# Optimization experiments

Measured on AMD Instinct MI355X. Metric: run time of the kernel, lower is better.

The kernel has to match this reference:

```python
import jax, jax.numpy as jnp
import numpy as np
import math

D_MODEL = 1024
D_STATE = 16
D_CONV = 4
EXPAND = 2
D_INNER = EXPAND * D_MODEL
DT_RANK = 64
BATCH = 4
SEQ_LEN = 2048


def setup_inputs() -> dict:
    key = jax.random.key(0)
    ks = jax.random.split(key, 10)
    hidden_states = jax.random.normal(ks[0], (BATCH, SEQ_LEN, D_MODEL), jnp.float32)
    in_proj_w = jax.random.normal(ks[1], (D_MODEL, 2 * D_INNER), jnp.float32) * (D_MODEL ** -0.5)
    conv_w = jax.random.normal(ks[2], (D_INNER, D_CONV), jnp.float32) * (D_CONV ** -0.5)
    conv_b = jnp.zeros((D_INNER,), jnp.float32)
    x_proj_w = jax.random.normal(ks[3], (D_INNER, DT_RANK + 2 * D_STATE), jnp.float32) * (D_INNER ** -0.5)
    dt_init_std = DT_RANK ** -0.5
    dt_proj_w = jax.random.uniform(ks[4], (DT_RANK, D_INNER), jnp.float32, -dt_init_std, dt_init_std)
    # inverse-softplus init of dt bias: dt ~ logUniform(dt_min, dt_max)
    dt_min, dt_max, dt_floor = 0.001, 0.1, 1e-4
    dt = jnp.exp(jax.random.uniform(ks[5], (D_INNER,), jnp.float32) * (math.log(dt_max) - math.log(dt_min)) + math.log(dt_min))
    dt = jnp.clip(dt, dt_floor, None)
    dt_proj_b = dt + jnp.log(-jnp.expm1(-dt))
    A = jnp.tile(jnp.arange(1, D_STATE + 1, dtype=jnp.float32)[None, :], (D_INNER, 1))
    A_log = jnp.log(A)
    D = jnp.ones((D_INNER,), jnp.float32)
    out_proj_w = jax.random.normal(ks[6], (D_INNER, D_MODEL), jnp.float32) * (D_INNER ** -0.5)
    return {
        "hidden_states": hidden_states,
        "in_proj_w": in_proj_w,
        "conv_w": conv_w,
        "conv_b": conv_b,
        "x_proj_w": x_proj_w,
        "dt_proj_w": dt_proj_w,
        "dt_proj_b": dt_proj_b,
        "A_log": A_log,
        "D": D,
        "out_proj_w": out_proj_w,
    }


def _mamba_forward(hidden_states, in_proj_w, conv_w, conv_b, x_proj_w, dt_proj_w, dt_proj_b, A_log, D, out_proj_w):
    b, L, _ = hidden_states.shape
    d_state = A_log.shape[1]
    dt_rank = dt_proj_w.shape[0]
    K = conv_w.shape[1]

    xz = hidden_states @ in_proj_w                     # (b, L, 2*d_inner)
    x, z = jnp.split(xz, 2, axis=-1)                   # each (b, L, d_inner)

    # causal depthwise conv1d (padding = K-1, truncated to L)
    x_pad = jnp.pad(x, ((0, 0), (K - 1, 0), (0, 0)))
    x = sum(x_pad[:, k:k + L, :] * conv_w[:, k] for k in range(K)) + conv_b
    x = jax.nn.silu(x)

    x_dbl = x @ x_proj_w                               # (b, L, dt_rank + 2*d_state)
    dt, B, C = jnp.split(x_dbl, [dt_rank, dt_rank + d_state], axis=-1)
    dt = jax.nn.softplus(dt @ dt_proj_w + dt_proj_b)   # (b, L, d_inner)
    A = -jnp.exp(A_log)                                # (d_inner, d_state)

    def step(h, inp):
        x_t, dt_t, B_t, C_t = inp                      # (b,d), (b,d), (b,n), (b,n)
        dA = jnp.exp(A[None] * dt_t[..., None])        # (b, d, n)
        h = dA * h + dt_t[..., None] * B_t[:, None, :] * x_t[..., None]
        y_t = jnp.einsum('bdn,bn->bd', h, C_t) + D * x_t
        return h, y_t

    h0 = jnp.zeros((b, x.shape[-1], d_state), x.dtype)
    xs = (x.transpose(1, 0, 2), dt.transpose(1, 0, 2), B.transpose(1, 0, 2), C.transpose(1, 0, 2))
    _, ys = jax.lax.scan(step, h0, xs)                 # ys: (L, b, d_inner)
    y = ys.transpose(1, 0, 2) * jax.nn.silu(z)
    return y @ out_proj_w                              # (b, L, d_model)


def reference(hidden_states, in_proj_w, conv_w, conv_b, x_proj_w, dt_proj_w, dt_proj_b, A_log, D, out_proj_w):
    return _mamba_forward(hidden_states, in_proj_w, conv_w, conv_b, x_proj_w, dt_proj_w, dt_proj_b, A_log, D, out_proj_w)
```

## Files before the change

### kernel.cpp

```cpp
#include <hip/hip_runtime.h>
#include <hip/hip_bf16.h>


#define DM 1024
#define DS 16
#define DC 4
#define DI 2048
#define DR 64
#define NB 4
#define SL 2048
#define NTOK (NB*SL)
#define XDBL_W (DR + 2*DS)
#define CONV_R 8

typedef __hip_bfloat16 bf16;
typedef unsigned short u16;
typedef __attribute__((ext_vector_type(8))) short s8v;
typedef __attribute__((ext_vector_type(4))) float f4v;
typedef __attribute__((ext_vector_type(2))) float f2v;
typedef __attribute__((ext_vector_type(4))) unsigned short us4;

__device__ __forceinline__ float b2f(bf16 v) { return __bfloat162float(v); }
__device__ __forceinline__ bf16  f2b(float v) { return __float2bfloat16(v); }
__device__ __forceinline__ u16 f2u(float x) {
    union { bf16 h; u16 s; } u; u.h = f2b(x); return u.s;
}
__device__ __forceinline__ float u2f(u16 s) {
    union { bf16 h; u16 s; } u; u.s = s; return b2f(u.h);
}

__device__ __forceinline__ bool sniff_bf16(const void* Dones) {
    return ((const u16*)Dones)[0] == 0x3F80u;
}

__device__ __forceinline__ float softplus_fast(float v) {
    return fmaxf(v, 0.f) + __logf(1.f + __expf(-fabsf(v)));
}

__device__ __forceinline__ float silu_fast(float v) {
    return v * __builtin_amdgcn_rcpf(1.f + __expf(-v));
}

template<int MODE>
__device__ __forceinline__ float ld(const void* p, size_t i, bool bf) {
    if (MODE == 0) return b2f(((const bf16*)p)[i]);
    if (MODE == 1) return ((const float*)p)[i];
    return bf ? b2f(((const bf16*)p)[i]) : ((const float*)p)[i];
}
template<int MODE>
__device__ __forceinline__ void st(void* p, size_t i, bool bf, float v) {
    if (MODE == 0)      { ((bf16*)p)[i] = f2b(v); }
    else if (MODE == 1) { ((float*)p)[i] = v; }
    else { if (bf) ((bf16*)p)[i] = f2b(v); else ((float*)p)[i] = v; }
}

template<int CM>
__device__ __forceinline__ void cstore(void* C, void* C2, size_t m, int n,
                                       int ldc, bool bf, float v) {
    if (CM == 3) {
        if (n < DR) ((bf16*)C2)[m * DR + n] = f2b(v);
        else        ((float*)C)[m * (2 * DS) + (n - DR)] = v;
    } else {
        st<CM>(C, m * (size_t)ldc + n, bf, v);
    }
}

#define AS1 __attribute__((address_space(1)))
#define AS3 __attribute__((address_space(3)))
__device__ __forceinline__ void gload_lds16(const void* g, void* l) {
    __builtin_amdgcn_global_load_lds((const AS1 unsigned int*)g,
                                     (AS3 unsigned int*)l, 16, 0, 0);
}

__global__ __launch_bounds__(256) void cast_bf16_kernel(
    const void* __restrict__ src, bf16* __restrict__ dst,
    const void* __restrict__ sniff)
{
    const bool bf = sniff_bf16(sniff);
    const size_t i = ((size_t)blockIdx.x * 256 + threadIdx.x) * 4;
    if (bf) {
        *(us4*)((u16*)dst + i) = *(const us4*)((const u16*)src + i);
    } else {
        const f4v f = *(const f4v*)((const float*)src + i);
        us4 o; o.x = f2u(f.x); o.y = f2u(f.y); o.z = f2u(f.z); o.w = f2u(f.w);
        *(us4*)((u16*)dst + i) = o;
    }
}

__global__ __launch_bounds__(256) void transpose_w(
    const void* __restrict__ w, bf16* __restrict__ wt,
    int K, int N, const void* __restrict__ sniff)
{
    const bool bf = sniff_bf16(sniff);
    __shared__ float t[32][33];
    const int tx = threadIdx.x & 31, ty = threadIdx.x >> 5;
    const int n0 = blockIdx.x * 32, k0 = blockIdx.y * 32;
    #pragma unroll
    for (int i = 0; i < 4; i++) {
        int k = k0 + ty + i * 8, n = n0 + tx;
        t[ty + i * 8][tx] = (n < N) ? ld<2>(w, (size_t)k * N + n, bf) : 0.f;
    }
    __syncthreads();
    #pragma unroll
    for (int i = 0; i < 4; i++) {
        int n = n0 + ty + i * 8, k = k0 + tx;
        wt[(size_t)n * K + k] = f2b(t[tx][ty + i * 8]);
    }
}

template<int BN, int CM>
__global__ __launch_bounds__(512, 1) void gemm_big(
    const bf16* __restrict__ A, int lda,
    const bf16* __restrict__ Bt,
    void* __restrict__ C, int ldc, int K,
    const void* __restrict__ sniff)
{
    constexpr int NF = BN / 128;
    constexpr int BH_ROWS = BN / 2;
    constexpr int BPASS = BH_ROWS / 64;
    constexpr int AH_B = 128 * 128;
    constexpr int BH_B = BH_ROWS * 128;

    const bool bf = sniff_bf16(sniff);
    __shared__ char AhL[2 * 2 * AH_B];
    __shared__ char BhL[2 * 2 * BH_B];

    const int tid = threadIdx.x, lane = tid & 63, wave = tid >> 6;
    const int wm = wave >> 2, wn = wave & 3;
    const int ll = lane & 15, qd = lane >> 4;
    const int swz = (ll & 7) << 4;

    const int m0 = blockIdx.x * 256, n0 = blockIdx.y * BN;

    const int s_r  = tid >> 3;
    const int s_cb = ((tid & 7) << 4) ^ ((s_r & 7) << 4);
    const char* Ab = (const char*)A;
    const char* Bb = (const char*)Bt;

#define STAGE_A(tt, hh) do {                                                  \
    char* _d = AhL + ((((tt) & 1) * 2 + (hh)) * AH_B);                        \
    _Pragma("unroll")                                                         \
    for (int _c = 0; _c < 2; ++_c) {                                          \
        const int _r = _c * 64 + s_r;                                         \
        gload_lds16(Ab + (((size_t)(m0 + (hh)*128 + _r) * lda + (tt)*64) << 1)\
                        + s_cb,                                               \
                    _d + _r * 128 + (tid & 7) * 16);                          \
    } } while (0)

#define STAGE_B(tt, hh) do {                                                  \
    char* _d = BhL + ((((tt) & 1) * 2 + (hh)) * BH_B);                        \
    _Pragma("unroll")                                                         \
    for (int _c = 0; _c < BPASS; ++_c) {                                      \
        const int _r = _c * 64 + s_r;                                         \
        gload_lds16(Bb + (((size_t)(n0 + (hh)*BH_ROWS + _r) * K + (tt)*64) << 1)\
                        + s_cb,                                               \
                    _d + _r * 128 + (tid & 7) * 16);                          \
    } } while (0)

#define WAIT_VC() do {                                                        \
    if constexpr (NF == 2) asm volatile("s_waitcnt vmcnt(4)" ::: "memory");   \
    else                   asm volatile("s_waitcnt vmcnt(3)" ::: "memory");   \
    } while (0)

    f4v acc[8][2 * NF];
    #pragma unroll
    for (int i = 0; i < 8; i++)
        #pragma unroll
        for (int j = 0; j < 2 * NF; j++) acc[i][j] = (f4v){0.f, 0.f, 0.f, 0.f};

    const int NT = K >> 6;
    STAGE_A(0, 0); STAGE_B(0, 0); STAGE_A(0, 1); STAGE_B(0, 1);
    STAGE_A(1, 0); STAGE_B(1, 0);
    WAIT_VC();
    __builtin_amdgcn_sched_barrier(0);
    __builtin_amdgcn_s_barrier();

    for (int t = 0; t < NT; ++t) {
        const int cur = t & 1;
        #pragma unroll
        for (int p = 0; p < 4; ++p) {
            const int mh = p >> 1, nh = p & 1;
            const char* Ah = AhL + (cur * 2 + mh) * AH_B;
            const char* Bh = BhL + (cur * 2 + nh) * BH_B;
            s8v af[4][2], bv[NF][2];
            #pragma unroll
            for (int fr = 0; fr < 4; ++fr)
                #pragma unroll
                for (int ks = 0; ks < 2; ++ks)
                    af[fr][ks] = *(const s8v*)(Ah + (wm*64 + fr*16 + ll) * 128
                                                  + ((ks*64 + qd*16) ^ swz));
            #pragma unroll
            for (int fn = 0; fn < NF; ++fn)
                #pragma unroll
                for (int ks = 0; ks < 2; ++ks)
                    bv[fn][ks] = *(const s8v*)(Bh + (wn*16*NF + fn*16 + ll) * 128
                                                  + ((ks*64 + qd*16) ^ swz));
            if (p == 0 && t + 1 < NT) STAGE_B(t + 1, 1);
            if (p == 1 && t + 1 < NT) STAGE_A(t + 1, 1);
            if (p == 2 && t + 2 < NT) STAGE_A(t + 2, 0);
            if (p == 3 && t + 2 < NT) STAGE_B(t + 2, 0);
            __builtin_amdgcn_sched_barrier(0);
            __builtin_amdgcn_s_barrier();
            asm volatile("s_waitcnt lgkmcnt(0)" ::: "memory");
            __builtin_amdgcn_sched_barrier(0);
            __builtin_amdgcn_s_setprio(1);
            #pragma unroll
            for (int fr = 0; fr < 4; ++fr)
                #pragma unroll
                for (int fn = 0; fn < NF; ++fn)
                    #pragma unroll
                    for (int ks = 0; ks < 2; ++ks)
                        acc[mh*4 + fr][nh*NF + fn] =
                            __builtin_amdgcn_mfma_f32_16x16x32_bf16(
                                af[fr][ks], bv[fn][ks],
                                acc[mh*4 + fr][nh*NF + fn], 0, 0, 0);
            __builtin_amdgcn_s_setprio(0);
            if (p == 3) WAIT_VC();
            __builtin_amdgcn_sched_barrier(0);
            __builtin_amdgcn_s_barrier();
        }
    }

    #pragma unroll
    for (int mh = 0; mh < 2; ++mh)
        #pragma unroll
        for (int fr = 0; fr < 4; ++fr)
            #pragma unroll
            for (int nh = 0; nh < 2; ++nh)
                #pragma unroll
                for (int fn = 0; fn < NF; ++fn) {
                    const int col = n0 + nh * (BN/2) + wn * 16 * NF + fn * 16 + ll;
                    #pragma unroll
                    for (int rr = 0; rr < 4; ++rr) {
                        const int row = m0 + mh * 128 + wm * 64 + fr * 16 + qd * 4 + rr;
                        st<CM>(C, (size_t)row * ldc + col, bf,
                               acc[mh*4 + fr][nh*NF + fn][rr]);
                    }
                }
#undef STAGE_A
#undef STAGE_B
#undef WAIT_VC
}

template<int CM, int EPI>
__global__ __launch_bounds__(256) void gemm_mfma(
    const bf16* __restrict__ A, int lda,
    const bf16* __restrict__ Bt,
    void* __restrict__ C, void* __restrict__ C2, int ldc,
    int M, int N, int K,
    const void* __restrict__ bias,
    const void* __restrict__ sniff)
{
    const bool bf = sniff_bf16(sniff);
    __shared__ short As[128 * 32];
    __shared__ short Bs[128 * 32];

    const int tid  = threadIdx.x;
    const int lane = tid & 63;
    const int wave = tid >> 6;
    const int wm = (wave & 1) * 64;
    const int wn = (wave >> 1) * 64;
    const int m0 = blockIdx.x * 128;
    const int n0 = blockIdx.y * 128;
    const int ll = lane & 15;
    const int qd = lane >> 4;

    const int srow  = lane >> 2;
    const int skoff = (lane & 3) * 8;

    const short* Ag = (const short*)A;
    const short* Bg = (const short*)Bt;
    char* AsB = (char*)As + wave * 2048 + lane * 16;
    char* BsB = (char*)Bs + wave * 2048 + lane * 16;
    const size_t a_row = (size_t)(m0 + wave * 32 + srow);
    const size_t b_row = (size_t)(n0 + wave * 32 + srow);

    f4v acc[4][4];
    #pragma unroll
    for (int i = 0; i < 4; i++)
        #pragma unroll
        for (int j = 0; j < 4; j++)
            acc[i][j] = (f4v){0.f, 0.f, 0.f, 0.f};

    for (int k0 = 0; k0 < K; k0 += 32) {
        gload_lds16(Ag + a_row * lda + k0 + skoff,            AsB);
        gload_lds16(Ag + (a_row + 16) * lda + k0 + skoff,     AsB + 1024);
        gload_lds16(Bg + b_row * K + k0 + skoff,              BsB);
        gload_lds16(Bg + (b_row + 16) * K + k0 + skoff,       BsB + 1024);
        __syncthreads();

        s8v af[4], bfr[4];
        #pragma unroll
        for (int s = 0; s < 4; s++)
            af[s] = *(const s8v*)&As[(wm + s * 16 + ll) * 32 + qd * 8];
        #pragma unroll
        for (int s = 0; s < 4; s++)
            bfr[s] = *(const s8v*)&Bs[(wn + s * 16 + ll) * 32 + qd * 8];
        #pragma unroll
        for (int i = 0; i < 4; i++)
            #pragma unroll
            for (int j = 0; j < 4; j++)
                acc[i][j] = __builtin_amdgcn_mfma_f32_16x16x32_bf16(
                    af[i], bfr[j], acc[i][j], 0, 0, 0);
        __syncthreads();
    }

    #pragma unroll
    for (int sn = 0; sn < 4; sn++) {
        const int cn = n0 + wn + sn * 16 + ll;
        if (cn >= N) continue;
        float bvv = 0.f;
        if (EPI == 1) bvv = ld<2>(bias, cn, bf);
        #pragma unroll
        for (int sm = 0; sm < 4; sm++) {
            #pragma unroll
            for (int r = 0; r < 4; r++) {
                const int cm = m0 + wm + sm * 16 + qd * 4 + r;
                float v = acc[sm][sn][r];
                if (EPI == 1) v = softplus_fast(v + bvv);
                cstore<CM>(C, C2, (size_t)cm, cn, ldc, bf, v);
            }
        }
    }
}

template<int AM, int CM, int EPI>
__global__ __launch_bounds__(256) void gemm_kernel(
    const void* __restrict__ A, int lda,
    const void* __restrict__ B, size_t bbase, int ldb,
    void* __restrict__ C, void* __restrict__ C2, int ldc,
    int M, int N, int K,
    const void* __restrict__ bias,
    const void* __restrict__ sniff)
{
    const bool bf = sniff_bf16(sniff);
    const int BM = 64, BN = 64, BK = 16;
    __shared__ float Asm[BK][BM + 4];
    __shared__ float Bsm[BK][BN + 4];

    const int tid = threadIdx.x;
    const int m0 = blockIdx.x * BM;
    const int n0 = blockIdx.y * BN;
    const int tx = tid % 16;
    const int ty = tid / 16;
    const int a_k = tid % BK;
    const int a_m = tid / BK;
    const int b_n = tid % BN;
    const int b_k = tid / BN;

    float acc[4][4] = {};

    for (int k0 = 0; k0 < K; k0 += BK) {
        #pragma unroll
        for (int i = 0; i < 4; i++) {
            int m = m0 + a_m + i * 16;
            float v = 0.f;
            if (m < M) v = ld<AM>(A, (size_t)m * lda + (k0 + a_k), bf);
            Asm[a_k][a_m + i * 16] = v;
        }
        #pragma unroll
        for (int i = 0; i < 4; i++) {
            int kk = b_k + i * 4;
            int n = n0 + b_n;
            float v = 0.f;
            if (n < N) v = ld<2>(B, bbase + (size_t)(k0 + kk) * ldb + n, bf);
            Bsm[kk][b_n] = v;
        }
        __syncthreads();
        #pragma unroll
        for (int kk = 0; kk < BK; kk++) {
            float av[4], bv[4];
            #pragma unroll
            for (int i = 0; i < 4; i++) av[i] = Asm[kk][ty * 4 + i];
            #pragma unroll
            for (int j = 0; j < 4; j++) bv[j] = Bsm[kk][tx * 4 + j];
            #pragma unroll
            for (int i = 0; i < 4; i++)
                #pragma unroll
                for (int j = 0; j < 4; j++)
                    acc[i][j] += av[i] * bv[j];
        }
        __syncthreads();
    }
    #pragma unroll
    for (int i = 0; i < 4; i++) {
        int m = m0 + ty * 4 + i;
        if (m >= M) continue;
        #pragma unroll
        for (int j = 0; j < 4; j++) {
            int n = n0 + tx * 4 + j;
            if (n >= N) continue;
            float v = acc[i][j];
            if (EPI == 1) {
                v += ld<2>(bias, n, bf);
                v = softplus_fast(v);
            }
            cstore<CM>(C, C2, (size_t)m, n, ldc, bf, v);
        }
    }
}

__global__ __launch_bounds__(256) void conv_silu_kernel(
    const bf16* __restrict__ xg, const void* __restrict__ w,
    const void* __restrict__ bias, bf16* __restrict__ xc,
    const void* __restrict__ sniff)
{
    const bool bf = sniff_bf16(sniff);
    const int c  = blockIdx.x * 256 + threadIdx.x;
    const int r0 = blockIdx.y * CONV_R;
    const int l0 = r0 % SL;

    float w0, w1, w2, w3;
    if (bf) {
        const us4 wv = *(const us4*)((const u16*)w + (size_t)c * 4);
        w0 = u2f(wv.x); w1 = u2f(wv.y); w2 = u2f(wv.z); w3 = u2f(wv.w);
    } else {
        const f4v wv = *(const f4v*)((const float*)w + (size_t)c * 4);
        w0 = wv.x; w1 = wv.y; w2 = wv.z; w3 = wv.w;
    }
    const float bs = ld<2>(bias, c, bf);

    float xm3 = (l0 >= 3) ? b2f(xg[(size_t)(r0 - 3) * DI + c]) : 0.f;
    float xm2 = (l0 >= 2) ? b2f(xg[(size_t)(r0 - 2) * DI + c]) : 0.f;
    float xm1 = (l0 >= 1) ? b2f(xg[(size_t)(r0 - 1) * DI + c]) : 0.f;

    #pragma unroll
    for (int i = 0; i < CONV_R; i++) {
        const size_t row = (size_t)(r0 + i);
        const float x0 = b2f(xg[row * DI + c]);
        const float acc = bs + w0 * xm3 + w1 * xm2 + w2 * xm1 + w3 * x0;
        const float s = acc / (1.f + __expf(-acc));
        xc[row * DI + c] = f2b(s);
        xm3 = xm2; xm2 = xm1; xm1 = x0;
    }
}

__global__ __launch_bounds__(256) void scan_pass1(
    const bf16* __restrict__ xc, const bf16* __restrict__ dt,
    const float* __restrict__ bc,
    const void* __restrict__ A_log, const void* __restrict__ Dones,
    float* __restrict__ P, float* __restrict__ Q, int nch)
{
    const bool bf = sniff_bf16(Dones);
    const int tid = threadIdx.x;
    const int d = blockIdx.x * 256 + tid;
    const int c = blockIdx.y;
    const int b = blockIdx.z;
    const int T = SL / nch;
    __shared__ u16 xs[32 * 256];
    __shared__ u16 ts[32 * 256];
    __shared__ float bcs[32 * 2 * DS];

    const size_t base = (size_t)b * SL + (size_t)c * T;
    const int lane = tid & 63, wv = tid >> 6;
    const int d0 = blockIdx.x * 256;
    const u16* xg16 = (const u16*)xc + base * DI + d0;
    const u16* tg16 = (const u16*)dt + base * DI + d0;
    for (int k = wv; k < (T >> 1); k += 4) {
        const int row = (k << 1) + (lane >> 5);
        const int c8  = (lane & 31) * 8;
        gload_lds16(xg16 + (size_t)row * DI + c8, (char*)xs + k * 1024 + lane * 16);
        gload_lds16(tg16 + (size_t)row * DI + c8, (char*)ts + k * 1024 + lane * 16);
    }
    const u16* bc16 = (const u16*)(bc + base * (2 * DS));
    for (int k = wv; k < (T >> 3); k += 4)
        gload_lds16(bc16 + k * 512 + lane * 8, (char*)bcs + k * 1024 + lane * 16);

    float a[DS];
    bool lad = true;
    #pragma unroll
    for (int n = 0; n < DS; n++) {
        a[n] = -__expf(ld<2>(A_log, (size_t)d * DS + n, bf));
        lad = lad && (fabsf(a[n] - (n + 1) * a[0]) < 1e-3f);
    }
    __syncthreads();

    float Pp[DS], Qq[DS];
    if (lad) {
        const float a0 = a[0];
        float R = 1.f;
        f2v q2[8];
        #pragma unroll
        for (int j = 0; j < 8; j++) q2[j] = (f2v){0.f, 0.f};
        for (int i = 0; i < T; i++) {
            const float xv = u2f(xs[i * 256 + tid]);
            const float tv = u2f(ts[i * 256 + tid]);
            const float dtx = tv * xv;
            const f4v* B4 = (const f4v*)&bcs[i * 2 * DS];
            const float r = __expf(a0 * tv);
            const float r2 = r * r, r4 = r2 * r2;
            const f2v r4v = {r4, r4};
            f2v cA = {r, r2};
            f2v cB = {r2 * r, r4};
            const f2v dtx2 = {dtx, dtx};
            R *= r;
            #pragma unroll
            for (int j4 = 0; j4 < 4; j4++) {
                const f4v Bq = B4[j4];
                const f2v b0 = {Bq.x, Bq.y}, b1 = {Bq.z, Bq.w};
                q2[2 * j4]     = cA * q2[2 * j4]     + dtx2 * b0;
                q2[2 * j4 + 1] = cB * q2[2 * j4 + 1] + dtx2 * b1;
                cA *= r4v; cB *= r4v;
            }
        }
        const float R2 = R * R, R3 = R2 * R, R4 = R2 * R2;
        float pa = R, pb = R2, pc = R3, pd = R4;
        #pragma unroll
        for (int n = 0; n < DS; n += 4) {
            Pp[n] = pa; Pp[n + 1] = pb; Pp[n + 2] = pc; Pp[n + 3] = pd;
            pa *= R4; pb *= R4; pc *= R4; pd *= R4;
        }
        #pragma unroll
        for (int j = 0; j < 8; j++) { Qq[2 * j] = q2[j].x; Qq[2 * j + 1] = q2[j].y; }
    } else {
        #pragma unroll
        for (int n = 0; n < DS; n++) { Pp[n] = 1.f; Qq[n] = 0.f; }
        for (int i = 0; i < T; i++) {
            const float xv = u2f(xs[i * 256 + tid]);
            const float tv = u2f(ts[i * 256 + tid]);
            const float dtx = tv * xv;
            const float* Bv = &bcs[i * 2 * DS];
            #pragma unroll
            for (int n = 0; n < DS; n++) {
                const float dA = __expf(a[n] * tv);
                Pp[n] *= dA;
                Qq[n] = dA * Qq[n] + dtx * Bv[n];
            }
        }
    }
    const size_t ob = ((size_t)b * nch + c) * (DS * DI) + d;
    #pragma unroll
    for (int n = 0; n < DS; n++) {
        P[ob + (size_t)n * DI] = Pp[n];
        Q[ob + (size_t)n * DI] = Qq[n];
    }
}

__global__ __launch_bounds__(256) void scan_pass2(
    float* __restrict__ P, const float* __restrict__ Q, int nch)
{
    const int j = blockIdx.x * 256 + threadIdx.x;
    const int b = blockIdx.y;
    float h = 0.f;
    for (int c = 0; c < nch; c++) {
        const size_t o = ((size_t)b * nch + c) * (DI * DS) + j;
        const float p = P[o];
        const float q = Q[o];
        P[o] = h;
        h = p * h + q;
    }
}

__global__ __launch_bounds__(256) void scan_pass3(
    const bf16* __restrict__ xc, const bf16* __restrict__ dt,
    const float* __restrict__ bc, bf16* __restrict__ z,
    const void* __restrict__ A_log, const void* __restrict__ Dones,
    const float* __restrict__ H, int nch)
{
    const bool bf = sniff_bf16(Dones);
    const int tid = threadIdx.x;
    const int d = blockIdx.x * 256 + tid;
    const int c = blockIdx.y;
    const int b = blockIdx.z;
    const int T = SL / nch;
    __shared__ u16 xs[32 * 256];
    __shared__ u16 ts[32 * 256];
    __shared__ u16 zs[32 * 256];
    __shared__ float bcs[32 * 2 * DS];

    const size_t base = (size_t)b * SL + (size_t)c * T;
    const int lane = tid & 63, wv = tid >> 6;
    const int d0 = blockIdx.x * 256;
    const u16* xg16 = (const u16*)xc + base * DI + d0;
    const u16* tg16 = (const u16*)dt + base * DI + d0;
    const u16* zg16 = (const u16*)z + base * DI + d0;
    for (int k = wv; k < (T >> 1); k += 4) {
        const int row = (k << 1) + (lane >> 5);
        const int c8  = (lane & 31) * 8;
        gload_lds16(xg16 + (size_t)row * DI + c8, (char*)xs + k * 1024 + lane * 16);
        gload_lds16(tg16 + (size_t)row * DI + c8, (char*)ts + k * 1024 + lane * 16);
        gload_lds16(zg16 + (size_t)row * DI + c8, (char*)zs + k * 1024 + lane * 16);
    }
    const u16* bc16 = (const u16*)(bc + base * (2 * DS));
    for (int k = wv; k < (T >> 3); k += 4)
        gload_lds16(bc16 + k * 512 + lane * 8, (char*)bcs + k * 1024 + lane * 16);

    float a[DS];
    bool lad = true;
    const size_t ob = ((size_t)b * nch + c) * (DS * DI) + d;
    #pragma unroll
    for (int n = 0; n < DS; n++) {
        a[n] = -__expf(ld<2>(A_log, (size_t)d * DS + n, bf));
        lad = lad && (fabsf(a[n] - (n + 1) * a[0]) < 1e-3f);
    }
    const float dD = ld<2>(Dones, d, bf);
    u16* zp = (u16*)z + base * DI + d;
    __syncthreads();

    if (lad) {
        const float a0 = a[0];
        f2v h2[8];
        #pragma unroll
        for (int j = 0; j < 8; j++)
            h2[j] = (f2v){H[ob + (size_t)(2 * j) * DI],
                          H[ob + (size_t)(2 * j + 1) * DI]};
        for (int i = 0; i < T; i++) {
            const float xv = u2f(xs[i * 256 + tid]);
            const float tv = u2f(ts[i * 256 + tid]);
            const float zv = u2f(zs[i * 256 + tid]);
            const float dtx = tv * xv;
            const f4v* B4 = (const f4v*)&bcs[i * 2 * DS];
            const f4v* C4 = B4 + 4;
            const float r = __expf(a0 * tv);
            const float r2 = r * r, r4 = r2 * r2;
            const f2v r4v = {r4, r4};
            f2v cA = {r, r2};
            f2v cB = {r2 * r, r4};
            const f2v dtx2 = {dtx, dtx};
            f2v ya = {dD * xv, 0.f}, yb = {0.f, 0.f};
            #pragma unroll
            for (int j4 = 0; j4 < 4; j4++) {
                const f4v Bq = B4[j4], Cq = C4[j4];
                const f2v b0 = {Bq.x, Bq.y}, b1 = {Bq.z, Bq.w};
                const f2v c0 = {Cq.x, Cq.y}, c1 = {Cq.z, Cq.w};
                h2[2 * j4]     = cA * h2[2 * j4]     + dtx2 * b0;
                ya += h2[2 * j4] * c0;
                h2[2 * j4 + 1] = cB * h2[2 * j4 + 1] + dtx2 * b1;
                yb += h2[2 * j4 + 1] * c1;
                cA *= r4v; cB *= r4v;
            }
            const float y = (ya.x + ya.y) + (yb.x + yb.y);
            zp[(size_t)i * DI] = f2u(y * silu_fast(zv));
        }
    } else {
        float h[DS];
        #pragma unroll
        for (int n = 0; n < DS; n++) h[n] = H[ob + (size_t)n * DI];
        for (int i = 0; i < T; i++) {
            const float xv = u2f(xs[i * 256 + tid]);
            const float tv = u2f(ts[i * 256 + tid]);
            const float zv = u2f(zs[i * 256 + tid]);
            const float dtx = tv * xv;
            const float* Bv = &bcs[i * 2 * DS];
            const float* Cv = Bv + DS;
            float y = dD * xv;
            #pragma unroll
            for (int n = 0; n < DS; n++) {
                const float dA = __expf(a[n] * tv);
                h[n] = dA * h[n] + dtx * Bv[n];
                y += h[n] * Cv[n];
            }
            zp[(size_t)i * DI] = f2u(y * silu_fast(zv));
        }
    }
}

__global__ __launch_bounds__(256) void scan_serial(
    const bf16* __restrict__ xc, const bf16* __restrict__ dt,
    const float* __restrict__ bc, bf16* __restrict__ z,
    const void* __restrict__ A_log, const void* __restrict__ Dones)
{
    const bool bf = sniff_bf16(Dones);
    const int d = blockIdx.x * 256 + threadIdx.x;
    const int b = blockIdx.y;
    float a[DS], h[DS];
    #pragma unroll
    for (int n = 0; n < DS; n++) {
        a[n] = -__expf(ld<2>(A_log, (size_t)d * DS + n, bf));
        h[n] = 0.f;
    }
    const float dD = ld<2>(Dones, d, bf);
    const size_t base = (size_t)b * SL;
    for (int l = 0; l < SL; l++) {
        const size_t row = base + l;
        const float xv  = b2f(xc[row * DI + d]);
        const float dtv = b2f(dt[row * DI + d]);
        const float* Bv = bc + row * (2 * DS);
        const float dtx = dtv * xv;
        float y = dD * xv;
        #pragma unroll
        for (int n = 0; n < DS; n++) {
            const float dA = __expf(a[n] * dtv);
            h[n] = dA * h[n] + dtx * Bv[n];
            y += h[n] * Bv[DS + n];
        }
        const float zv = b2f(z[row * DI + d]);
        const float g = zv / (1.f + __expf(-zv));
        z[row * DI + d] = f2b(y * g);
    }
}

extern "C" void kernel_launch(void* const* d_in, const int* in_sizes, int n_in,
                              void* d_out, int out_size, void* d_ws, size_t ws_size,
                              hipStream_t stream) {
    const void* hs        = d_in[0];
    const void* in_proj_w = d_in[1];
    const void* conv_w    = d_in[2];
    const void* conv_b    = d_in[3];
    const void* x_proj_w  = d_in[4];
    const void* dt_proj_w = d_in[5];
    const void* dt_proj_b = d_in[6];
    const void* A_log     = d_in[7];
    const void* Dones     = d_in[8];
    const void* out_proj_w= d_in[9];

    char* ws = (char*)d_ws;
    bf16*  xg   = (bf16*)(ws);
    bf16*  xc   = (bf16*)(ws + 33554432);
    bf16*  hsb  = (bf16*)(ws + 33554432);
    bf16*  z    = (bf16*)(ws + 67108864);
    float* bc   = (float*)(ws + 100663296);
    bf16*  dtf  = (bf16*)(ws + 101711872);
    const size_t WT_OFF = 102760448;
    bf16* in_projT  = (bf16*)(ws + WT_OFF);
    bf16* x_projT   = (bf16*)(ws + WT_OFF);
    bf16* dt_projT  = (bf16*)(ws + WT_OFF + 524288);
    bf16* out_projT = (bf16*)(ws + WT_OFF);
    const bool mfma_ok = ws_size >= WT_OFF + 8388608;

    const size_t per_chunk = (size_t)NB * DI * DS * 4 * 2;
    int nch = 64;
    while (nch > 1 && WT_OFF + (size_t)nch * per_chunk > ws_size) nch >>= 1;
    const bool chunked = (nch >= 64) &&
                         (WT_OFF + (size_t)nch * per_chunk <= ws_size);
    float* P = (float*)(ws + WT_OFF);
    float* Q = P + (size_t)NB * nch * DI * DS;

    bf16* dtb = xg;

    if (mfma_ok) {
        cast_bf16_kernel<<<(NTOK*DM/4)/256, 256, 0, stream>>>(hs, hsb, Dones);
        transpose_w<<<dim3((2*DI)/32, DM/32), 256, 0, stream>>>(
            in_proj_w, in_projT, DM, 2*DI, Dones);
        gemm_big<256, 0><<<dim3(NTOK/256, DI/256), 512, 0, stream>>>(
            hsb, DM, in_projT, xg, DI, DM, Dones);
        gemm_big<256, 0><<<dim3(NTOK/256, DI/256), 512, 0, stream>>>(
            hsb, DM, in_projT + (size_t)DI * DM, z, DI, DM, Dones);
        conv_silu_kernel<<<dim3(DI/256, NTOK/CONV_R), 256, 0, stream>>>(
            xg, conv_w, conv_b, xc, Dones);
        transpose_w<<<dim3(128/32, DI/32), 256, 0, stream>>>(
            x_proj_w, x_projT, DI, XDBL_W, Dones);
        gemm_mfma<3, 0><<<dim3(NTOK/128, 1), 256, 0, stream>>>(
            xc, DI, x_projT, bc, dtf, 0, NTOK, XDBL_W, DI, nullptr, Dones);
        transpose_w<<<dim3(DI/32, DR/32), 256, 0, stream>>>(
            dt_proj_w, dt_projT, DR, DI, Dones);
        gemm_mfma<0, 1><<<dim3(NTOK/128, DI/128), 256, 0, stream>>>(
            dtf, DR, dt_projT, dtb, nullptr, DI, NTOK, DI, DR, dt_proj_b, Dones);
    } else {
        gemm_kernel<2, 0, 0><<<dim3(NTOK/64, DI/64), 256, 0, stream>>>(
            hs, DM, in_proj_w, 0, 2*DI, xg, nullptr, DI, NTOK, DI, DM, nullptr, Dones);
        gemm_kernel<2, 0, 0><<<dim3(NTOK/64, DI/64), 256, 0, stream>>>(
            hs, DM, in_proj_w, DI, 2*DI, z, nullptr, DI, NTOK, DI, DM, nullptr, Dones);
        conv_silu_kernel<<<dim3(DI/256, NTOK/CONV_R), 256, 0, stream>>>(
            xg, conv_w, conv_b, xc, Dones);
        gemm_kernel<0, 3, 0><<<dim3(NTOK/64, (XDBL_W + 63)/64), 256, 0, stream>>>(
            xc, DI, x_proj_w, 0, XDBL_W, bc, dtf, 0, NTOK, XDBL_W, DI, nullptr, Dones);
        gemm_kernel<0, 0, 1><<<dim3(NTOK/64, DI/64), 256, 0, stream>>>(
            dtf, DR, dt_proj_w, 0, DI, dtb, nullptr, DI, NTOK, DI, DR, dt_proj_b, Dones);
    }

    if (chunked) {
        scan_pass1<<<dim3(DI/256, nch, NB), 256, 0, stream>>>(
            xc, dtb, bc, A_log, Dones, P, Q, nch);
        scan_pass2<<<dim3((DI*DS)/256, NB), 256, 0, stream>>>(P, Q, nch);
        scan_pass3<<<dim3(DI/256, nch, NB), 256, 0, stream>>>(
            xc, dtb, bc, z, A_log, Dones, P, nch);
    } else {
        scan_serial<<<dim3(DI/256, NB), 256, 0, stream>>>(
            xc, dtb, bc, z, A_log, Dones);
    }

    if (mfma_ok) {
        transpose_w<<<dim3(DM/32, DI/32), 256, 0, stream>>>(
            out_proj_w, out_projT, DI, DM, Dones);
        gemm_big<128, 2><<<dim3(NTOK/256, DM/128), 512, 0, stream>>>(
            z, DI, out_projT, d_out, DM, DI, Dones);
    } else {
        gemm_kernel<0, 2, 0><<<dim3(NTOK/64, DM/64), 256, 0, stream>>>(
            z, DI, out_proj_w, 0, DM, d_out, nullptr, DM, NTOK, DM, DI, nullptr, Dones);
    }
}
```

Before: 450.2 us.

## Use 256x128 tiles with a three-slot rotating LDS buffer in big GEMM

The big GEMM kernel is narrowed to a single 256x128 tile shape, so the in_proj GEMMs now also use BN=128 and launch twice as many blocks. The double-buffered LDS (four halves) is replaced by a three-slot ring indexed by (2t+h)%3, with prefetch of the next K-tile spread across the four phases and new vmcnt waits. Launch bounds rise to 4 blocks per CU in the hint. The goal is to cut LDS and register use so more blocks fit per CU and latency hides better. The cost is less data reuse per tile and a shallower prefetch distance.

```diff
diff --git a/kernel.cpp b/kernel.cpp
--- a/kernel.cpp
+++ b/kernel.cpp
@@ -108,37 +108,36 @@
     }
 }
 
-template<int BN, int CM>
-__global__ __launch_bounds__(512, 1) void gemm_big(
+template<int CM>
+__global__ __launch_bounds__(512, 4) void gemm_big(
     const bf16* __restrict__ A, int lda,
     const bf16* __restrict__ Bt,
     void* __restrict__ C, int ldc, int K,
     const void* __restrict__ sniff)
 {
-    constexpr int NF = BN / 128;
-    constexpr int BH_ROWS = BN / 2;
-    constexpr int BPASS = BH_ROWS / 64;
     constexpr int AH_B = 128 * 128;
-    constexpr int BH_B = BH_ROWS * 128;
+    constexpr int BH_B = 64 * 128;
 
     const bool bf = sniff_bf16(sniff);
-    __shared__ char AhL[2 * 2 * AH_B];
-    __shared__ char BhL[2 * 2 * BH_B];
+    __shared__ char AhL[3 * AH_B];
+    __shared__ char BhL[3 * BH_B];
 
     const int tid = threadIdx.x, lane = tid & 63, wave = tid >> 6;
     const int wm = wave >> 2, wn = wave & 3;
     const int ll = lane & 15, qd = lane >> 4;
     const int swz = (ll & 7) << 4;
 
-    const int m0 = blockIdx.x * 256, n0 = blockIdx.y * BN;
+    const int m0 = blockIdx.x * 256, n0 = blockIdx.y * 128;
 
     const int s_r  = tid >> 3;
     const int s_cb = ((tid & 7) << 4) ^ ((s_r & 7) << 4);
     const char* Ab = (const char*)A;
     const char* Bb = (const char*)Bt;
 
+#define ASLOT(tt, hh) (((2 * (tt) + (hh)) % 3))
+
 #define STAGE_A(tt, hh) do {                                                  \
-    char* _d = AhL + ((((tt) & 1) * 2 + (hh)) * AH_B);                        \
+    char* _d = AhL + ASLOT(tt, hh) * AH_B;                                    \
     _Pragma("unroll")                                                         \
     for (int _c = 0; _c < 2; ++_c) {                                          \
         const int _r = _c * 64 + s_r;                                         \
@@ -148,41 +147,34 @@
     } } while (0)
 
 #define STAGE_B(tt, hh) do {                                                  \
-    char* _d = BhL + ((((tt) & 1) * 2 + (hh)) * BH_B);                        \
-    _Pragma("unroll")                                                         \
-    for (int _c = 0; _c < BPASS; ++_c) {                                      \
-        const int _r = _c * 64 + s_r;                                         \
-        gload_lds16(Bb + (((size_t)(n0 + (hh)*BH_ROWS + _r) * K + (tt)*64) << 1)\
+    char* _d = BhL + ASLOT(tt, hh) * BH_B;                                    \
+    {                                                                         \
+        const int _r = s_r;                                                   \
+        gload_lds16(Bb + (((size_t)(n0 + (hh)*64 + _r) * K + (tt)*64) << 1)   \
                         + s_cb,                                               \
                     _d + _r * 128 + (tid & 7) * 16);                          \
     } } while (0)
 
-#define WAIT_VC() do {                                                        \
-    if constexpr (NF == 2) asm volatile("s_waitcnt vmcnt(4)" ::: "memory");   \
-    else                   asm volatile("s_waitcnt vmcnt(3)" ::: "memory");   \
-    } while (0)
-
-    f4v acc[8][2 * NF];
+    f4v acc[8][2];
     #pragma unroll
     for (int i = 0; i < 8; i++)
         #pragma unroll
-        for (int j = 0; j < 2 * NF; j++) acc[i][j] = (f4v){0.f, 0.f, 0.f, 0.f};
+        for (int j = 0; j < 2; j++) acc[i][j] = (f4v){0.f, 0.f, 0.f, 0.f};
 
     const int NT = K >> 6;
     STAGE_A(0, 0); STAGE_B(0, 0); STAGE_A(0, 1); STAGE_B(0, 1);
-    STAGE_A(1, 0); STAGE_B(1, 0);
-    WAIT_VC();
+    asm volatile("s_waitcnt vmcnt(3)" ::: "memory");
     __builtin_amdgcn_sched_barrier(0);
     __builtin_amdgcn_s_barrier();
 
     for (int t = 0; t < NT; ++t) {
-        const int cur = t & 1;
+        const bool more = (t + 1 < NT);
         #pragma unroll
         for (int p = 0; p < 4; ++p) {
             const int mh = p >> 1, nh = p & 1;
-            const char* Ah = AhL + (cur * 2 + mh) * AH_B;
-            const char* Bh = BhL + (cur * 2 + nh) * BH_B;
-            s8v af[4][2], bv[NF][2];
+            const char* Ah = AhL + ASLOT(t, mh) * AH_B;
+            const char* Bh = BhL + ASLOT(t, nh) * BH_B;
+            s8v af[4][2], bv[2];
             #pragma unroll
             for (int fr = 0; fr < 4; ++fr)
                 #pragma unroll
@@ -190,15 +182,14 @@
                     af[fr][ks] = *(const s8v*)(Ah + (wm*64 + fr*16 + ll) * 128
                                                   + ((ks*64 + qd*16) ^ swz));
             #pragma unroll
-            for (int fn = 0; fn < NF; ++fn)
-                #pragma unroll
-                for (int ks = 0; ks < 2; ++ks)
-                    bv[fn][ks] = *(const s8v*)(Bh + (wn*16*NF + fn*16 + ll) * 128
-                                                  + ((ks*64 + qd*16) ^ swz));
-            if (p == 0 && t + 1 < NT) STAGE_B(t + 1, 1);
-            if (p == 1 && t + 1 < NT) STAGE_A(t + 1, 1);
-            if (p == 2 && t + 2 < NT) STAGE_A(t + 2, 0);
-            if (p == 3 && t + 2 < NT) STAGE_B(t + 2, 0);
+            for (int ks = 0; ks < 2; ++ks)
+                bv[ks] = *(const s8v*)(Bh + (wn*16 + ll) * 128
+                                          + ((ks*64 + qd*16) ^ swz));
+            if (more) {
+                if (p == 0) { STAGE_A(t + 1, 0); STAGE_B(t + 1, 0); }
+                if (p == 2) { STAGE_A(t + 1, 1); }
+                if (p == 3) { STAGE_B(t + 1, 1); }
+            }
             __builtin_amdgcn_sched_barrier(0);
             __builtin_amdgcn_s_barrier();
             asm volatile("s_waitcnt lgkmcnt(0)" ::: "memory");
@@ -207,15 +198,17 @@
             #pragma unroll
             for (int fr = 0; fr < 4; ++fr)
                 #pragma unroll
-                for (int fn = 0; fn < NF; ++fn)
-                    #pragma unroll
-                    for (int ks = 0; ks < 2; ++ks)
-                        acc[mh*4 + fr][nh*NF + fn] =
-                            __builtin_amdgcn_mfma_f32_16x16x32_bf16(
-                                af[fr][ks], bv[fn][ks],
-                                acc[mh*4 + fr][nh*NF + fn], 0, 0, 0);
+                for (int ks = 0; ks < 2; ++ks)
+                    acc[mh*4 + fr][nh] =
+                        __builtin_amdgcn_mfma_f32_16x16x32_bf16(
+                            af[fr][ks], bv[ks], acc[mh*4 + fr][nh], 0, 0, 0);
             __builtin_amdgcn_s_setprio(0);
-            if (p == 3) WAIT_VC();
+            if (p == 0) {
+                if (more) asm volatile("s_waitcnt vmcnt(3)" ::: "memory");
+                else      asm volatile("s_waitcnt vmcnt(0)" ::: "memory");
+            }
+            if (p == 3 && more)
+                asm volatile("s_waitcnt vmcnt(3)" ::: "memory");
             __builtin_amdgcn_sched_barrier(0);
             __builtin_amdgcn_s_barrier();
         }
@@ -226,20 +219,18 @@
         #pragma unroll
         for (int fr = 0; fr < 4; ++fr)
             #pragma unroll
-            for (int nh = 0; nh < 2; ++nh)
+            for (int nh = 0; nh < 2; ++nh) {
+                const int col = n0 + nh * 64 + wn * 16 + ll;
                 #pragma unroll
-                for (int fn = 0; fn < NF; ++fn) {
-                    const int col = n0 + nh * (BN/2) + wn * 16 * NF + fn * 16 + ll;
-                    #pragma unroll
-                    for (int rr = 0; rr < 4; ++rr) {
-                        const int row = m0 + mh * 128 + wm * 64 + fr * 16 + qd * 4 + rr;
-                        st<CM>(C, (size_t)row * ldc + col, bf,
-                               acc[mh*4 + fr][nh*NF + fn][rr]);
-                    }
+                for (int rr = 0; rr < 4; ++rr) {
+                    const int row = m0 + mh * 128 + wm * 64 + fr * 16 + qd * 4 + rr;
+                    st<CM>(C, (size_t)row * ldc + col, bf,
+                           acc[mh*4 + fr][nh][rr]);
                 }
+            }
 #undef STAGE_A
 #undef STAGE_B
-#undef WAIT_VC
+#undef ASLOT
 }
 
 template<int CM, int EPI>
@@ -732,9 +723,9 @@
         cast_bf16_kernel<<<(NTOK*DM/4)/256, 256, 0, stream>>>(hs, hsb, Dones);
         transpose_w<<<dim3((2*DI)/32, DM/32), 256, 0, stream>>>(
             in_proj_w, in_projT, DM, 2*DI, Dones);
-        gemm_big<256, 0><<<dim3(NTOK/256, DI/256), 512, 0, stream>>>(
+        gemm_big<0><<<dim3(NTOK/256, DI/128), 512, 0, stream>>>(
             hsb, DM, in_projT, xg, DI, DM, Dones);
-        gemm_big<256, 0><<<dim3(NTOK/256, DI/256), 512, 0, stream>>>(
+        gemm_big<0><<<dim3(NTOK/256, DI/128), 512, 0, stream>>>(
             hsb, DM, in_projT + (size_t)DI * DM, z, DI, DM, Dones);
         conv_silu_kernel<<<dim3(DI/256, NTOK/CONV_R), 256, 0, stream>>>(
             xg, conv_w, conv_b, xc, Dones);
@@ -773,7 +764,7 @@
     if (mfma_ok) {
         transpose_w<<<dim3(DM/32, DI/32), 256, 0, stream>>>(
             out_proj_w, out_projT, DI, DM, Dones);
-        gemm_big<128, 2><<<dim3(NTOK/256, DM/128), 512, 0, stream>>>(
+        gemm_big<2><<<dim3(NTOK/256, DM/128), 512, 0, stream>>>(
             z, DI, out_projT, d_out, DM, DI, Dones);
     } else {
         gemm_kernel<0, 2, 0><<<dim3(NTOK/64, DM/64), 256, 0, stream>>>(
```

Result: slower. 638.1 us (+41.8%).
